# Kernel tuning notes

Measured on AMD Instinct MI355X. Metric: run time of the kernel, lower is better.

Reference implementation:

```python
import jax, jax.numpy as jnp
import numpy as np

DIM = 1024
HID = 2816  # int(2*4096/3)=2730 rounded up to multiple of 256
E = 2       # n_modalities
N = 32768   # tokens
EPS = 1e-5


def setup_inputs() -> dict:
    key = jax.random.key(0)
    ks = jax.random.split(key, 6)
    x = jax.random.normal(ks[0], (N, DIM), jnp.float32)
    # per-token modality label -> disjoint boolean masks [E, N]
    labels = jax.random.randint(ks[1], (N,), 0, E)
    modality_masks = labels[None, :] == jnp.arange(E)[:, None]
    s_in = 1.0 / np.sqrt(DIM)
    s_hid = 1.0 / np.sqrt(HID)
    # nn.Linear stores weight as [out_features, in_features]
    w1 = jax.random.normal(ks[2], (E, HID, DIM), jnp.float32) * s_in
    w3 = jax.random.normal(ks[3], (E, HID, DIM), jnp.float32) * s_in
    w2 = jax.random.normal(ks[4], (E, DIM, HID), jnp.float32) * s_hid
    norm_w = jnp.ones((E, DIM), jnp.float32)
    return {"x": x, "modality_masks": modality_masks,
            "w1": w1, "w3": w3, "w2": w2, "norm_w": norm_w}


def reference(x, modality_masks, w1, w3, w2, norm_w):
    # Each expert: SwiGLU FFN followed by RMSNorm (computed in fp32).
    def expert(W1, W3, W2, g):
        h = jax.nn.silu(x @ W1.T) * (x @ W3.T)   # [N, HID]
        o = h @ W2.T                              # [N, DIM]
        of = o.astype(jnp.float32)
        n = of * jax.lax.rsqrt(jnp.mean(of * of, axis=-1, keepdims=True) + EPS)
        return (n * g.astype(jnp.float32)).astype(o.dtype)

    outs = jax.vmap(expert)(w1, w3, w2, norm_w)   # [E, N, DIM]
    merged = jnp.zeros_like(x)
    for i in range(E - 1, -1, -1):
        merged = jnp.where(modality_masks[i][:, None], outs[i], merged)
    return merged
```

## Files before the change

kernel.cpp:

```cpp
#include <hip/hip_runtime.h>
#include <stdint.h>

#define DIM   1024
#define HID   2816
#define NEXP  2
#define NTOK  32768
#define RMS_EPS 1e-5f
#define NK1   16
#define NK2   44
#define NNT1  22
#define NNT2  4

typedef unsigned short u16;
typedef unsigned int   u32;
typedef __bf16 bf16_t;
typedef bf16_t bf16x8 __attribute__((ext_vector_type(8)));
typedef float  f32x4  __attribute__((ext_vector_type(4)));

#define BAR() asm volatile("s_barrier" ::: "memory")
#define WAIT6() asm volatile("s_waitcnt vmcnt(6)" ::: "memory")
#define WAIT0() asm volatile("s_waitcnt vmcnt(0)" ::: "memory")
#define MFMA_(a,b,c) __builtin_amdgcn_mfma_f32_16x16x32_bf16(a, b, c, 0, 0, 0)

__device__ __forceinline__ u16 f2bf(float f) {
  u32 u = __float_as_uint(f);
  u += 0x7FFFu + ((u >> 16) & 1u);
  return (u16)(u >> 16);
}

__device__ __forceinline__ void gld16(void* lds, const void* g) {
  __builtin_amdgcn_global_load_lds(
      (__attribute__((address_space(1))) void*)g,
      (__attribute__((address_space(3))) void*)lds, 16, 0, 0);
}

__device__ __forceinline__ int detect_layout(const u32* mi) {
  const int lane = threadIdx.x & 63;
  bool all01 = true, allf = true;
  for (int j = 0; j < 8; ++j) {
    u32 w = mi[j * 64 + lane];
    all01 &= (w <= 1u);
    allf  &= (w == 0u || w == 0x3F800000u);
  }
  unsigned long long b01 = __ballot(all01);
  unsigned long long bfl = __ballot(allf);
  if (b01 == ~0ull) return 0;
  if (bfl == ~0ull) return 1;
  return 2;
}

__device__ __forceinline__ bool mask_at(const void* m, int layout, int e, int n) {
  if (layout == 0) return ((const u32*)m)[e * NTOK + n] != 0u;
  if (layout == 1) return ((const float*)m)[e * NTOK + n] != 0.f;
  return ((const unsigned char*)m)[e * NTOK + n] != 0;
}

__device__ __forceinline__ int label_of(const void* m, int layout, int n) {
  for (int e = 0; e < NEXP; ++e)
    if (mask_at(m, layout, e, n)) return e;
  return 0;
}

__global__ __launch_bounds__(1024) void k_setup(const void* __restrict__ masks,
                                                int* __restrict__ meta,
                                                int* __restrict__ idx) {
  const int layout = detect_layout((const u32*)masks);
  const int t = threadIdx.x;
  const int base_n = t << 5;
  u32 bits = 0; int c0 = 0;
  for (int j = 0; j < 32; ++j) {
    const int l_ = label_of(masks, layout, base_n + j);
    bits |= ((u32)l_) << j;
    c0 += 1 - l_;
  }
  int inc = c0;
#pragma unroll
  for (int d = 1; d < 64; d <<= 1) {
    int v = __shfl_up(inc, d, 64);
    if ((t & 63) >= d) inc += v;
  }
  __shared__ int wsum[16];
  __shared__ int wexc[17];
  const int wv = t >> 6, ln = t & 63;
  if (ln == 63) wsum[wv] = inc;
  __syncthreads();
  if (t == 0) {
    int a = 0;
    for (int w = 0; w < 16; ++w) { wexc[w] = a; a += wsum[w]; }
    wexc[16] = a;
  }
  __syncthreads();
  const int cnt0 = wexc[16];
  int p0 = wexc[wv] + inc - c0;
  int p1 = cnt0 + base_n - p0;
  for (int j = 0; j < 32; ++j) {
    const int n = base_n + j;
    if ((bits >> j) & 1u) idx[p1++] = n;
    else                  idx[p0++] = n;
  }
  if (t == 0) { meta[0] = cnt0; meta[1] = NTOK - cnt0; }
}

__global__ void k_cvt(const float* __restrict__ in, u16* __restrict__ out, int n4) {
  const int stride = gridDim.x * blockDim.x;
  for (int i = blockIdx.x * blockDim.x + threadIdx.x; i < n4; i += stride) {
    const float4 v = ((const float4*)in)[i];
    ushort4 o;
    o.x = f2bf(v.x); o.y = f2bf(v.y); o.z = f2bf(v.z); o.w = f2bf(v.w);
    ((ushort4*)out)[i] = o;
  }
}

__global__ __launch_bounds__(256) void k_cvtx(const float* __restrict__ x,
                                              const int* __restrict__ idx,
                                              u16* __restrict__ xg) {
  const int r = blockIdx.x;
  const int tok = idx[r];
  const float4 v = ((const float4*)(x + ((size_t)tok << 10)))[threadIdx.x];
  ushort4 o;
  o.x = f2bf(v.x); o.y = f2bf(v.y); o.z = f2bf(v.z); o.w = f2bf(v.w);
  ((ushort4*)(xg + ((size_t)r << 10)))[threadIdx.x] = o;
}


#define ST1A(BUF, HH, P_, KT) {                                        \
    char* _d = (char*)&sA[BUF][(HH) * 8192] + t * 16;                  \
    gld16(_d,        ((HH) ? P_.a2 : P_.a0) + (size_t)(KT) * 64);      \
    gld16(_d + 8192, ((HH) ? P_.a3 : P_.a1) + (size_t)(KT) * 64); }

#define ST1B(BUF, HH, P_, KT) {                                                 \
    gld16((char*)&sB1[BUF][(HH) * 4096] + t * 16,                               \
          ((HH) ? P_.b11 : P_.b10) + (size_t)(KT) * 64);                        \
    gld16((char*)&sB3[BUF][(HH) * 4096] + t * 16,                               \
          ((HH) ? P_.b31 : P_.b30) + (size_t)(KT) * 64); }

#define G1_PH(MQ, NQ, ...) {                                                   \
    if ((MQ) == 0 && (NQ) == 0) {                                              \
      _Pragma("unroll") for (int q_ = 0; q_ < 2; ++q_) {                       \
        b1f0[q_] = *(const bf16x8*)&sB1c[bBase + q_*4096 + kb0];               \
        b1f1[q_] = *(const bf16x8*)&sB1c[bBase + q_*4096 + kb1];               \
        b3f0[q_] = *(const bf16x8*)&sB3c[bBase + q_*4096 + kb0];               \
        b3f1[q_] = *(const bf16x8*)&sB3c[bBase + q_*4096 + kb1];               \
      }                                                                        \
    }                                                                          \
    if ((NQ) == 0) {                                                           \
      _Pragma("unroll") for (int mi = 0; mi < 4; ++mi) {                       \
        af0[mi] = *(const bf16x8*)&sAc[aBase + (MQ)*8192 + mi*1024 + kb0];     \
        af1[mi] = *(const bf16x8*)&sAc[aBase + (MQ)*8192 + mi*1024 + kb1];     \
      }                                                                        \
    }                                                                          \
    __VA_ARGS__                                                                \
    BAR();                                                                     \
    __builtin_amdgcn_s_setprio(1);                                             \
    _Pragma("unroll") for (int mi = 0; mi < 4; ++mi) {                         \
      acc1[MQ][NQ][mi] = MFMA_(af0[mi], b1f0[NQ], acc1[MQ][NQ][mi]);           \
      acc3[MQ][NQ][mi] = MFMA_(af0[mi], b3f0[NQ], acc3[MQ][NQ][mi]);           \
      acc1[MQ][NQ][mi] = MFMA_(af1[mi], b1f1[NQ], acc1[MQ][NQ][mi]);           \
      acc3[MQ][NQ][mi] = MFMA_(af1[mi], b3f1[NQ], acc3[MQ][NQ][mi]);           \
    }                                                                          \
    __builtin_amdgcn_s_setprio(0);                                             \
  }

#define SETUP1(P_, IT) {                                                        \
    int _it = (IT);                                                            \
    int _m  = c + ((_it / NNT1) << 3);                                         \
    P_.nT   = _it % NNT1;                                                      \
    int _e  = _m >= nmt0;                                                      \
    P_.mT   = _e ? _m - nmt0 : _m;                                             \
    P_.cnt  = _e ? cnt1 : cnt0;                                                \
    P_.bas  = _e ? cnt0 : 0;                                                   \
    int _rg;                                                                   \
    _rg = P_.mT*256       + r0; _rg = _rg < P_.cnt ? _rg : P_.cnt-1;           \
    P_.a0 = xg + (size_t)(P_.bas+_rg)*DIM + srcoff;                            \
    _rg = P_.mT*256 +  64 + r0; _rg = _rg < P_.cnt ? _rg : P_.cnt-1;           \
    P_.a1 = xg + (size_t)(P_.bas+_rg)*DIM + srcoff;                            \
    _rg = P_.mT*256 + 128 + r0; _rg = _rg < P_.cnt ? _rg : P_.cnt-1;           \
    P_.a2 = xg + (size_t)(P_.bas+_rg)*DIM + srcoff;                            \
    _rg = P_.mT*256 + 192 + r0; _rg = _rg < P_.cnt ? _rg : P_.cnt-1;           \
    P_.a3 = xg + (size_t)(P_.bas+_rg)*DIM + srcoff;                            \
    size_t _o = ((size_t)_e * HID + (size_t)P_.nT * 128 + r0) * DIM + srcoff;  \
    P_.b10 = w1b + _o; P_.b11 = w1b + _o + (size_t)64 * DIM;                   \
    P_.b30 = w3b + _o; P_.b31 = w3b + _o + (size_t)64 * DIM; }

__global__ __launch_bounds__(512, 2) void k_gemm1(
    const u16* __restrict__ xg, const u16* __restrict__ w1b,
    const u16* __restrict__ w3b, const int* __restrict__ meta,
    u16* __restrict__ h)
{
  const int cnt0 = meta[0], cnt1 = meta[1];
  const int nmt0 = (cnt0 + 255) >> 8;
  const int nmt  = nmt0 + ((cnt1 + 255) >> 8);
  const int c = blockIdx.x & 7, q = blockIdx.x >> 3;
  const int mcnt  = (nmt > c) ? (((nmt - 1 - c) >> 3) + 1) : 0;
  const int items = mcnt * NNT1;
  int i = q;
  if (i >= items) return;

  __shared__ __attribute__((aligned(16))) u16 sA [2][256 * 64];
  __shared__ __attribute__((aligned(16))) u16 sB1[2][128 * 64];
  __shared__ __attribute__((aligned(16))) u16 sB3[2][128 * 64];

  const int t = threadIdx.x;
  const int srcoff = ((t & 7) ^ ((t >> 3) & 7)) * 8;
  const int r0 = t >> 3;
  const int wid = t >> 6, l = t & 63;
  const int wr = wid >> 2, wc = wid & 3;
  const int l15 = l & 15, lk = l >> 4, l7 = l & 7;
  const int kb0 = ((0 + lk) ^ l7) * 8;
  const int kb1 = ((4 + lk) ^ l7) * 8;
  const int aBase = (wr * 64 + l15) * 64;
  const int bBase = (wc * 16 + l15) * 64;

  struct P { const u16 *a0,*a1,*a2,*a3,*b10,*b11,*b30,*b31; int mT,cnt,bas,nT; };
  P cur, nxt;
  SETUP1(cur, i)
  bool hasN = (i + 32) < items;
  if (hasN) { SETUP1(nxt, i + 32) } else { nxt = cur; }

  f32x4 acc1[2][2][4] = {};
  f32x4 acc3[2][2][4] = {};
  bf16x8 af0[4], af1[4];
  bf16x8 b1f0[2], b1f1[2], b3f0[2], b3f1[2];

  ST1A(0, 0, cur, 0) ST1A(0, 1, cur, 0) ST1B(0, 0, cur, 0) ST1B(0, 1, cur, 0)
  ST1A(1, 0, cur, 1) ST1A(1, 1, cur, 1) ST1B(1, 0, cur, 1)
  WAIT6();
  BAR();

  for (;;) {
#pragma unroll 2
    for (int k = 0; k < NK1 - 2; ++k) {
      const u16* sAc  = &sA [k & 1][0];
      const u16* sB1c = &sB1[k & 1][0];
      const u16* sB3c = &sB3[k & 1][0];
      G1_PH(0, 0, ST1B((k & 1) ^ 1, 1, cur, k + 1))
      BAR();
      G1_PH(0, 1, ST1A(k & 1, 0, cur, k + 2))
      BAR();
      G1_PH(1, 0, )
      BAR();
      G1_PH(1, 1, ST1A(k & 1, 1, cur, k + 2) ST1B(k & 1, 0, cur, k + 2))
      WAIT6();
      BAR();
    }
    {
      const u16* sAc  = &sA [0][0];
      const u16* sB1c = &sB1[0][0];
      const u16* sB3c = &sB3[0][0];
      G1_PH(0, 0, ST1B(1, 1, cur, 15))
      BAR();
      G1_PH(0, 1, if (hasN) ST1A(0, 0, nxt, 0))
      BAR();
      G1_PH(1, 0, )
      BAR();
      G1_PH(1, 1, if (hasN) { ST1A(0, 1, nxt, 0) ST1B(0, 0, nxt, 0) })
      if (hasN) WAIT6(); else WAIT0();
      BAR();
    }
    {
      const u16* sAc  = &sA [1][0];
      const u16* sB1c = &sB1[1][0];
      const u16* sB3c = &sB3[1][0];
      G1_PH(0, 0, if (hasN) ST1B(0, 1, nxt, 0))
      BAR();
      G1_PH(0, 1, if (hasN) ST1A(1, 0, nxt, 1))
      BAR();
      G1_PH(1, 0, )
      BAR();
      G1_PH(1, 1, if (hasN) { ST1A(1, 1, nxt, 1) ST1B(1, 0, nxt, 1) })
      if (hasN) WAIT6();
      BAR();
    }

#pragma unroll
    for (int mq = 0; mq < 2; ++mq)
#pragma unroll
      for (int mi = 0; mi < 4; ++mi)
#pragma unroll
        for (int r = 0; r < 4; ++r) {
          const int lrow = mq * 128 + wr * 64 + mi * 16 + lk * 4 + r;
          const int rg = cur.mT * 256 + lrow;
          if (rg < cur.cnt) {
            u16* hrow = h + (size_t)(cur.bas + rg) * HID + cur.nT * 128 + wc * 16 + l15;
#pragma unroll
            for (int nq = 0; nq < 2; ++nq) {
              const float a = acc1[mq][nq][mi][r];
              const float b = acc3[mq][nq][mi][r];
              hrow[nq * 64] = f2bf((a / (1.f + __expf(-a))) * b);
            }
          }
        }

    if (!hasN) break;
    cur = nxt;
    i += 32;
    hasN = (i + 32) < items;
    if (hasN) SETUP1(nxt, i + 32)
#pragma unroll
    for (int a_ = 0; a_ < 2; ++a_)
#pragma unroll
      for (int b_ = 0; b_ < 2; ++b_)
#pragma unroll
        for (int m_ = 0; m_ < 4; ++m_) {
          acc1[a_][b_][m_] = (f32x4){0.f, 0.f, 0.f, 0.f};
          acc3[a_][b_][m_] = (f32x4){0.f, 0.f, 0.f, 0.f};
        }
  }
}


#define ST2A(BUF, HH, P_, KT) {                                        \
    char* _d = (char*)&sA[BUF][(HH) * 8192] + t * 16;                  \
    gld16(_d,        ((HH) ? P_.a2 : P_.a0) + (size_t)(KT) * 64);      \
    gld16(_d + 8192, ((HH) ? P_.a3 : P_.a1) + (size_t)(KT) * 64); }

#define ST2B(BUF, HH, P_, KT) {                                        \
    char* _d = (char*)&sB[BUF][(HH) * 8192] + t * 16;                  \
    gld16(_d,        ((HH) ? P_.b2 : P_.b0) + (size_t)(KT) * 64);      \
    gld16(_d + 8192, ((HH) ? P_.b3 : P_.b1) + (size_t)(KT) * 64); }

#define G2_PH(MQ, NQ, ...) {                                                   \
    if ((MQ) == 0 && (NQ) == 0) {                                              \
      _Pragma("unroll") for (int q_ = 0; q_ < 2; ++q_)                         \
        _Pragma("unroll") for (int ni = 0; ni < 2; ++ni) {                     \
          bf0[q_][ni] = *(const bf16x8*)&sBc[bBase + q_*8192 + ni*1024 + kb0]; \
          bf1[q_][ni] = *(const bf16x8*)&sBc[bBase + q_*8192 + ni*1024 + kb1]; \
        }                                                                      \
    }                                                                          \
    if ((NQ) == 0) {                                                           \
      _Pragma("unroll") for (int mi = 0; mi < 4; ++mi) {                       \
        af0[mi] = *(const bf16x8*)&sAc[aBase + (MQ)*8192 + mi*1024 + kb0];     \
        af1[mi] = *(const bf16x8*)&sAc[aBase + (MQ)*8192 + mi*1024 + kb1];     \
      }                                                                        \
    }                                                                          \
    __VA_ARGS__                                                                \
    BAR();                                                                     \
    __builtin_amdgcn_s_setprio(1);                                             \
    _Pragma("unroll") for (int mi = 0; mi < 4; ++mi)                           \
      _Pragma("unroll") for (int ni = 0; ni < 2; ++ni) {                       \
        acc[MQ][NQ][mi][ni] = MFMA_(af0[mi], bf0[NQ][ni], acc[MQ][NQ][mi][ni]);\
        acc[MQ][NQ][mi][ni] = MFMA_(af1[mi], bf1[NQ][ni], acc[MQ][NQ][mi][ni]);\
      }                                                                        \
    __builtin_amdgcn_s_setprio(0);                                             \
  }

#define SETUP2(P_, IT) {                                                        \
    int _it = (IT);                                                            \
    int _m  = c + ((_it >> 2) << 3);                                           \
    P_.nT   = _it & 3;                                                         \
    int _e  = _m >= nmt0;                                                      \
    P_.mT   = _e ? _m - nmt0 : _m;                                             \
    P_.cnt  = _e ? cnt1 : cnt0;                                                \
    P_.bas  = _e ? cnt0 : 0;                                                   \
    int _rg;                                                                   \
    _rg = P_.mT*256       + r0; _rg = _rg < P_.cnt ? _rg : P_.cnt-1;           \
    P_.a0 = hbuf + (size_t)(P_.bas+_rg)*HID + srcoff;                          \
    _rg = P_.mT*256 +  64 + r0; _rg = _rg < P_.cnt ? _rg : P_.cnt-1;           \
    P_.a1 = hbuf + (size_t)(P_.bas+_rg)*HID + srcoff;                          \
    _rg = P_.mT*256 + 128 + r0; _rg = _rg < P_.cnt ? _rg : P_.cnt-1;           \
    P_.a2 = hbuf + (size_t)(P_.bas+_rg)*HID + srcoff;                          \
    _rg = P_.mT*256 + 192 + r0; _rg = _rg < P_.cnt ? _rg : P_.cnt-1;           \
    P_.a3 = hbuf + (size_t)(P_.bas+_rg)*HID + srcoff;                          \
    size_t _wb = ((size_t)_e * DIM + (size_t)P_.nT * 256 + r0) * HID + srcoff; \
    P_.b0 = w2b + _wb;                                                         \
    P_.b1 = w2b + _wb + (size_t) 64 * HID;                                     \
    P_.b2 = w2b + _wb + (size_t)128 * HID;                                     \
    P_.b3 = w2b + _wb + (size_t)192 * HID; }

__global__ __launch_bounds__(512, 2) void k_gemm2(
    const u16* __restrict__ hbuf, const u16* __restrict__ w2b,
    const int* __restrict__ meta, const int* __restrict__ idx,
    float* __restrict__ out)
{
  const int cnt0 = meta[0], cnt1 = meta[1];
  const int nmt0 = (cnt0 + 255) >> 8;
  const int nmt  = nmt0 + ((cnt1 + 255) >> 8);
  const int c = blockIdx.x & 7, q = blockIdx.x >> 3;
  const int mcnt  = (nmt > c) ? (((nmt - 1 - c) >> 3) + 1) : 0;
  const int items = mcnt * NNT2;
  int i = q;
  if (i >= items) return;

  __shared__ __attribute__((aligned(16))) u16 sA[2][256 * 64];
  __shared__ __attribute__((aligned(16))) u16 sB[2][256 * 64];

  const int t = threadIdx.x;
  const int srcoff = ((t & 7) ^ ((t >> 3) & 7)) * 8;
  const int r0 = t >> 3;
  const int wid = t >> 6, l = t & 63;
  const int wr = wid >> 2, wc = wid & 3;
  const int l15 = l & 15, lk = l >> 4, l7 = l & 7;
  const int kb0 = ((0 + lk) ^ l7) * 8;
  const int kb1 = ((4 + lk) ^ l7) * 8;
  const int aBase = (wr * 64 + l15) * 64;
  const int bBase = (wc * 32 + l15) * 64;

  struct P { const u16 *a0,*a1,*a2,*a3,*b0,*b1,*b2,*b3; int mT,cnt,bas,nT; };
  P cur, nxt;
  SETUP2(cur, i)
  bool hasN = (i + 32) < items;
  if (hasN) { SETUP2(nxt, i + 32) } else { nxt = cur; }

  f32x4 acc[2][2][4][2] = {};
  bf16x8 af0[4], af1[4], bf0[2][2], bf1[2][2];

  ST2A(0, 0, cur, 0) ST2A(0, 1, cur, 0) ST2B(0, 0, cur, 0) ST2B(0, 1, cur, 0)
  ST2A(1, 0, cur, 1) ST2A(1, 1, cur, 1) ST2B(1, 0, cur, 1)
  WAIT6();
  BAR();

  for (;;) {
#pragma unroll 2
    for (int k = 0; k < NK2 - 2; ++k) {
      const u16* sAc = &sA[k & 1][0];
      const u16* sBc = &sB[k & 1][0];
      G2_PH(0, 0, ST2B((k & 1) ^ 1, 1, cur, k + 1))
      BAR();
      G2_PH(0, 1, ST2A(k & 1, 0, cur, k + 2))
      BAR();
      G2_PH(1, 0, )
      BAR();
      G2_PH(1, 1, ST2A(k & 1, 1, cur, k + 2) ST2B(k & 1, 0, cur, k + 2))
      WAIT6();
      BAR();
    }
    {
      const u16* sAc = &sA[0][0];
      const u16* sBc = &sB[0][0];
      G2_PH(0, 0, ST2B(1, 1, cur, NK2 - 1))
      BAR();
      G2_PH(0, 1, if (hasN) ST2A(0, 0, nxt, 0))
      BAR();
      G2_PH(1, 0, )
      BAR();
      G2_PH(1, 1, if (hasN) { ST2A(0, 1, nxt, 0) ST2B(0, 0, nxt, 0) })
      if (hasN) WAIT6(); else WAIT0();
      BAR();
    }
    {
      const u16* sAc = &sA[1][0];
      const u16* sBc = &sB[1][0];
      G2_PH(0, 0, if (hasN) ST2B(0, 1, nxt, 0))
      BAR();
      G2_PH(0, 1, if (hasN) ST2A(1, 0, nxt, 1))
      BAR();
      G2_PH(1, 0, )
      BAR();
      G2_PH(1, 1, if (hasN) { ST2A(1, 1, nxt, 1) ST2B(1, 0, nxt, 1) })
      if (hasN) WAIT6();
      BAR();
    }

#pragma unroll
    for (int mq = 0; mq < 2; ++mq)
#pragma unroll
      for (int mi = 0; mi < 4; ++mi)
#pragma unroll
        for (int r = 0; r < 4; ++r) {
          const int lrow = mq * 128 + wr * 64 + mi * 16 + lk * 4 + r;
          const int rg = cur.mT * 256 + lrow;
          if (rg < cur.cnt) {
            const int tok = idx[cur.bas + rg];
            float* orow = out + (size_t)tok * DIM + cur.nT * 256 + wc * 32 + l15;
#pragma unroll
            for (int nq = 0; nq < 2; ++nq)
#pragma unroll
              for (int ni = 0; ni < 2; ++ni)
                orow[nq * 128 + ni * 16] = acc[mq][nq][mi][ni][r];
          }
        }

    if (!hasN) break;
    cur = nxt;
    i += 32;
    hasN = (i + 32) < items;
    if (hasN) SETUP2(nxt, i + 32)
#pragma unroll
    for (int a_ = 0; a_ < 2; ++a_)
#pragma unroll
      for (int b_ = 0; b_ < 2; ++b_)
#pragma unroll
        for (int m_ = 0; m_ < 4; ++m_)
#pragma unroll
          for (int n_ = 0; n_ < 2; ++n_)
            acc[a_][b_][m_][n_] = (f32x4){0.f, 0.f, 0.f, 0.f};
  }
}

__global__ __launch_bounds__(256) void k_rms(
    float* __restrict__ out, const float* __restrict__ nw,
    const int* __restrict__ meta, const int* __restrict__ idx)
{
  const int wv = threadIdx.x >> 6, ln = threadIdx.x & 63;
  const int r = blockIdx.x * 4 + wv;
  const int e = (r >= meta[0]) ? 1 : 0;
  const int tok = idx[r];
  float* row = out + (size_t)tok * DIM;
  const float* g = nw + (size_t)e * DIM;

  float4 v[4];
  float ss = 0.f;
#pragma unroll
  for (int p = 0; p < 4; ++p) {
    v[p] = ((const float4*)row)[p * 64 + ln];
    ss += v[p].x * v[p].x + v[p].y * v[p].y + v[p].z * v[p].z + v[p].w * v[p].w;
  }
#pragma unroll
  for (int off = 32; off; off >>= 1) ss += __shfl_xor(ss, off, 64);
  const float sc = rsqrtf(ss * (1.0f / DIM) + RMS_EPS);
#pragma unroll
  for (int p = 0; p < 4; ++p) {
    const float4 gg = ((const float4*)g)[p * 64 + ln];
    v[p].x *= sc * gg.x; v[p].y *= sc * gg.y;
    v[p].z *= sc * gg.z; v[p].w *= sc * gg.w;
    ((float4*)row)[p * 64 + ln] = v[p];
  }
}

extern "C" void kernel_launch(void* const* d_in, const int* in_sizes, int n_in,
                              void* d_out, int out_size, void* d_ws, size_t ws_size,
                              hipStream_t stream)
{
  const float* x     = (const float*)d_in[0];
  const void*  masks = d_in[1];
  const float* w1    = (const float*)d_in[2];
  const float* w3    = (const float*)d_in[3];
  const float* w2    = (const float*)d_in[4];
  const float* nw    = (const float*)d_in[5];
  float* out = (float*)d_out;

  char* ws = (char*)d_ws;
  constexpr size_t OFF_IDX = 256;
  constexpr size_t OFF_XB  = OFF_IDX + (size_t)NTOK * 4;
  constexpr size_t OFF_W1B = OFF_XB + (size_t)NTOK * DIM * 2;
  constexpr size_t SZ_W    = (size_t)NEXP * HID * DIM * 2;
  constexpr size_t OFF_W3B = OFF_W1B + SZ_W;
  constexpr size_t OFF_W2B = OFF_W3B + SZ_W;
  constexpr size_t OFF_H   = OFF_W2B + SZ_W;

  int* meta = (int*)ws;
  int* idx  = (int*)(ws + OFF_IDX);
  u16* xg   = (u16*)(ws + OFF_XB);
  u16* w1b  = (u16*)(ws + OFF_W1B);
  u16* w3b  = (u16*)(ws + OFF_W3B);
  u16* w2b  = (u16*)(ws + OFF_W2B);
  u16* h    = (u16*)(ws + OFF_H);

  k_setup<<<1, 1024, 0, stream>>>(masks, meta, idx);

  const int wn4 = NEXP * HID * DIM / 4;
  k_cvt<<<2048, 256, 0, stream>>>(w1, w1b, wn4);
  k_cvt<<<2048, 256, 0, stream>>>(w3, w3b, wn4);
  k_cvt<<<2048, 256, 0, stream>>>(w2, w2b, wn4);
  k_cvtx<<<NTOK, 256, 0, stream>>>(x, idx, xg);

  k_gemm1<<<256, 512, 0, stream>>>(xg, w1b, w3b, meta, h);
  k_gemm2<<<256, 512, 0, stream>>>(h, w2b, meta, idx, out);
  k_rms<<<NTOK / 4, 256, 0, stream>>>(out, nw, meta, idx);
}
```

Measured before the change: 833.2 us.

## Switch both GEMMs to 32x32x16 MFMA with restructured fragment and prefetch schedule

Both grouped GEMM kernels now use the 32x32x16 bf16 MFMA instead of 16x16x32. The per-wave fragment layout, LDS read offsets, accumulator shapes and epilogue row/column mapping are rewritten to match. Global-to-LDS staging is split into quarter-tile loads spread across four phases, with adjusted vmcnt waits. The larger instruction is meant to cut MFMA issue count and LDS fragment reads per FLOP, at the cost of more accumulator registers and a riskier pipeline ordering.

```diff
diff --git a/kernel.cpp b/kernel.cpp
--- a/kernel.cpp
+++ b/kernel.cpp
@@ -15,12 +15,14 @@
 typedef unsigned int   u32;
 typedef __bf16 bf16_t;
 typedef bf16_t bf16x8 __attribute__((ext_vector_type(8)));
-typedef float  f32x4  __attribute__((ext_vector_type(4)));
-
-#define BAR() asm volatile("s_barrier" ::: "memory")
+typedef float  f32x16 __attribute__((ext_vector_type(16)));
+
+#define BAR()   asm volatile("s_barrier" ::: "memory")
+#define WAIT4() asm volatile("s_waitcnt vmcnt(4)" ::: "memory")
 #define WAIT6() asm volatile("s_waitcnt vmcnt(6)" ::: "memory")
+#define WAIT8() asm volatile("s_waitcnt vmcnt(8)" ::: "memory")
 #define WAIT0() asm volatile("s_waitcnt vmcnt(0)" ::: "memory")
-#define MFMA_(a,b,c) __builtin_amdgcn_mfma_f32_16x16x32_bf16(a, b, c, 0, 0, 0)
+#define M32(a,b,c) __builtin_amdgcn_mfma_f32_32x32x16_bf16(a, b, c, 0, 0, 0)
 
 __device__ __forceinline__ u16 f2bf(float f) {
   u32 u = __float_as_uint(f);
@@ -81,8 +83,8 @@
   }
   __shared__ int wsum[16];
   __shared__ int wexc[17];
-  const int wv = t >> 6, ln = t & 63;
-  if (ln == 63) wsum[wv] = inc;
+  const int wv = t >> 6;
+  if ((t & 63) == 63) wsum[wv] = inc;
   __syncthreads();
   if (t == 0) {
     int a = 0;
@@ -123,42 +125,53 @@
 }
 
 
-#define ST1A(BUF, HH, P_, KT) {                                        \
-    char* _d = (char*)&sA[BUF][(HH) * 8192] + t * 16;                  \
-    gld16(_d,        ((HH) ? P_.a2 : P_.a0) + (size_t)(KT) * 64);      \
-    gld16(_d + 8192, ((HH) ? P_.a3 : P_.a1) + (size_t)(KT) * 64); }
-
-#define ST1B(BUF, HH, P_, KT) {                                                 \
-    gld16((char*)&sB1[BUF][(HH) * 4096] + t * 16,                               \
-          ((HH) ? P_.b11 : P_.b10) + (size_t)(KT) * 64);                        \
-    gld16((char*)&sB3[BUF][(HH) * 4096] + t * 16,                               \
-          ((HH) ? P_.b31 : P_.b30) + (size_t)(KT) * 64); }
-
-#define G1_PH(MQ, NQ, ...) {                                                   \
-    if ((MQ) == 0 && (NQ) == 0) {                                              \
-      _Pragma("unroll") for (int q_ = 0; q_ < 2; ++q_) {                       \
-        b1f0[q_] = *(const bf16x8*)&sB1c[bBase + q_*4096 + kb0];               \
-        b1f1[q_] = *(const bf16x8*)&sB1c[bBase + q_*4096 + kb1];               \
-        b3f0[q_] = *(const bf16x8*)&sB3c[bBase + q_*4096 + kb0];               \
-        b3f1[q_] = *(const bf16x8*)&sB3c[bBase + q_*4096 + kb1];               \
-      }                                                                        \
-    }                                                                          \
-    if ((NQ) == 0) {                                                           \
-      _Pragma("unroll") for (int mi = 0; mi < 4; ++mi) {                       \
-        af0[mi] = *(const bf16x8*)&sAc[aBase + (MQ)*8192 + mi*1024 + kb0];     \
-        af1[mi] = *(const bf16x8*)&sAc[aBase + (MQ)*8192 + mi*1024 + kb1];     \
-      }                                                                        \
-    }                                                                          \
-    __VA_ARGS__                                                                \
-    BAR();                                                                     \
-    __builtin_amdgcn_s_setprio(1);                                             \
-    _Pragma("unroll") for (int mi = 0; mi < 4; ++mi) {                         \
-      acc1[MQ][NQ][mi] = MFMA_(af0[mi], b1f0[NQ], acc1[MQ][NQ][mi]);           \
-      acc3[MQ][NQ][mi] = MFMA_(af0[mi], b3f0[NQ], acc3[MQ][NQ][mi]);           \
-      acc1[MQ][NQ][mi] = MFMA_(af1[mi], b1f1[NQ], acc1[MQ][NQ][mi]);           \
-      acc3[MQ][NQ][mi] = MFMA_(af1[mi], b3f1[NQ], acc3[MQ][NQ][mi]);           \
-    }                                                                          \
-    __builtin_amdgcn_s_setprio(0);                                             \
+#define ST1A_Q(BUF, APTR, Q, KT) \
+    gld16((char*)&sA[BUF][(Q)*4096] + t*16, (APTR) + (size_t)(KT)*64);
+
+#define ST1B_H(BUF, HH, PB1, PB3, KT) {                                  \
+    gld16((char*)&sB1[BUF][(HH)*4096] + t*16, (PB1) + (size_t)(KT)*64);  \
+    gld16((char*)&sB3[BUF][(HH)*4096] + t*16, (PB3) + (size_t)(KT)*64); }
+
+#define G1_MFMA(RF, A0_, A1_, A2_, A3_)                                  \
+    acc1[RF] = M32(A0_, bh1[0], acc1[RF]);                               \
+    acc3[RF] = M32(A0_, bh3[0], acc3[RF]);                               \
+    acc1[RF] = M32(A1_, bh1[1], acc1[RF]);                               \
+    acc3[RF] = M32(A1_, bh3[1], acc3[RF]);                               \
+    acc1[RF] = M32(A2_, bh1[2], acc1[RF]);                               \
+    acc3[RF] = M32(A2_, bh3[2], acc3[RF]);                               \
+    acc1[RF] = M32(A3_, bh1[3], acc1[RF]);                               \
+    acc3[RF] = M32(A3_, bh3[3], acc3[RF]);
+
+#define G1_PH0(...) {                                                    \
+    bh1[0] = *(const bf16x8*)&sB1c[bb0];                                 \
+    bh1[1] = *(const bf16x8*)&sB1c[bb1];                                 \
+    bh1[2] = *(const bf16x8*)&sB1c[bb2];                                 \
+    bh1[3] = *(const bf16x8*)&sB1c[bb3];                                 \
+    bh3[0] = *(const bf16x8*)&sB3c[bb0];                                 \
+    bh3[1] = *(const bf16x8*)&sB3c[bb1];                                 \
+    bh3[2] = *(const bf16x8*)&sB3c[bb2];                                 \
+    bh3[3] = *(const bf16x8*)&sB3c[bb3];                                 \
+    bf16x8 a0_ = *(const bf16x8*)&sAc[av0];                              \
+    bf16x8 a1_ = *(const bf16x8*)&sAc[av1];                              \
+    bf16x8 a2_ = *(const bf16x8*)&sAc[av2];                              \
+    bf16x8 a3_ = *(const bf16x8*)&sAc[av3];                              \
+    __VA_ARGS__                                                          \
+    BAR();                                                               \
+    __builtin_amdgcn_s_setprio(1);                                       \
+    G1_MFMA(0, a0_, a1_, a2_, a3_)                                       \
+    __builtin_amdgcn_s_setprio(0);                                       \
+  }
+
+#define G1_PHX(RF, ...) {                                                \
+    bf16x8 a0_ = *(const bf16x8*)&sAc[av0 + (RF)*2048];                  \
+    bf16x8 a1_ = *(const bf16x8*)&sAc[av1 + (RF)*2048];                  \
+    bf16x8 a2_ = *(const bf16x8*)&sAc[av2 + (RF)*2048];                  \
+    bf16x8 a3_ = *(const bf16x8*)&sAc[av3 + (RF)*2048];                  \
+    __VA_ARGS__                                                          \
+    BAR();                                                               \
+    __builtin_amdgcn_s_setprio(1);                                       \
+    G1_MFMA(RF, a0_, a1_, a2_, a3_)                                      \
+    __builtin_amdgcn_s_setprio(0);                                       \
   }
 
 #define SETUP1(P_, IT) {                                                        \
@@ -205,11 +218,15 @@
   const int r0 = t >> 3;
   const int wid = t >> 6, l = t & 63;
   const int wr = wid >> 2, wc = wid & 3;
-  const int l15 = l & 15, lk = l >> 4, l7 = l & 7;
-  const int kb0 = ((0 + lk) ^ l7) * 8;
-  const int kb1 = ((4 + lk) ^ l7) * 8;
-  const int aBase = (wr * 64 + l15) * 64;
-  const int bBase = (wc * 16 + l15) * 64;
+  const int l31 = l & 31, h5 = l >> 5, l7 = l & 7;
+  const int ka0 = ((0 + h5) ^ l7) * 8;
+  const int ka1 = ((2 + h5) ^ l7) * 8;
+  const int ka2 = ((4 + h5) ^ l7) * 8;
+  const int ka3 = ((6 + h5) ^ l7) * 8;
+  const int aB = (wr * 128 + l31) * 64;
+  const int bB = (wc * 32 + l31) * 64;
+  const int av0 = aB + ka0, av1 = aB + ka1, av2 = aB + ka2, av3 = aB + ka3;
+  const int bb0 = bB + ka0, bb1 = bB + ka1, bb2 = bB + ka2, bb3 = bB + ka3;
 
   struct P { const u16 *a0,*a1,*a2,*a3,*b10,*b11,*b30,*b31; int mT,cnt,bas,nT; };
   P cur, nxt;
@@ -217,14 +234,16 @@
   bool hasN = (i + 32) < items;
   if (hasN) { SETUP1(nxt, i + 32) } else { nxt = cur; }
 
-  f32x4 acc1[2][2][4] = {};
-  f32x4 acc3[2][2][4] = {};
-  bf16x8 af0[4], af1[4];
-  bf16x8 b1f0[2], b1f1[2], b3f0[2], b3f1[2];
-
-  ST1A(0, 0, cur, 0) ST1A(0, 1, cur, 0) ST1B(0, 0, cur, 0) ST1B(0, 1, cur, 0)
-  ST1A(1, 0, cur, 1) ST1A(1, 1, cur, 1) ST1B(1, 0, cur, 1)
-  WAIT6();
+  f32x16 acc1[4] = {};
+  f32x16 acc3[4] = {};
+  bf16x8 bh1[4], bh3[4];
+
+  ST1B_H(0, 0, cur.b10, cur.b30, 0) ST1B_H(0, 1, cur.b11, cur.b31, 0)
+  ST1A_Q(0, cur.a0, 0, 0) ST1A_Q(0, cur.a1, 1, 0)
+  ST1A_Q(0, cur.a2, 2, 0) ST1A_Q(0, cur.a3, 3, 0)
+  ST1A_Q(1, cur.a0, 0, 1) ST1A_Q(1, cur.a2, 2, 1)
+  ST1B_H(1, 0, cur.b10, cur.b30, 1)
+  WAIT4();
   BAR();
 
   for (;;) {
@@ -233,13 +252,15 @@
       const u16* sAc  = &sA [k & 1][0];
       const u16* sB1c = &sB1[k & 1][0];
       const u16* sB3c = &sB3[k & 1][0];
-      G1_PH(0, 0, ST1B((k & 1) ^ 1, 1, cur, k + 1))
-      BAR();
-      G1_PH(0, 1, ST1A(k & 1, 0, cur, k + 2))
-      BAR();
-      G1_PH(1, 0, )
-      BAR();
-      G1_PH(1, 1, ST1A(k & 1, 1, cur, k + 2) ST1B(k & 1, 0, cur, k + 2))
+      const int cb = k & 1, nb = cb ^ 1;
+      G1_PH0(ST1B_H(nb, 1, cur.b11, cur.b31, k + 1))
+      BAR();
+      G1_PHX(1, ST1A_Q(nb, cur.a1, 1, k + 1) ST1A_Q(nb, cur.a3, 3, k + 1))
+      WAIT8();
+      BAR();
+      G1_PHX(2, ST1A_Q(cb, cur.a0, 0, k + 2) ST1A_Q(cb, cur.a2, 2, k + 2))
+      BAR();
+      G1_PHX(3, ST1B_H(cb, 0, cur.b10, cur.b30, k + 2))
       WAIT6();
       BAR();
     }
@@ -247,13 +268,14 @@
       const u16* sAc  = &sA [0][0];
       const u16* sB1c = &sB1[0][0];
       const u16* sB3c = &sB3[0][0];
-      G1_PH(0, 0, ST1B(1, 1, cur, 15))
-      BAR();
-      G1_PH(0, 1, if (hasN) ST1A(0, 0, nxt, 0))
-      BAR();
-      G1_PH(1, 0, )
-      BAR();
-      G1_PH(1, 1, if (hasN) { ST1A(0, 1, nxt, 0) ST1B(0, 0, nxt, 0) })
+      G1_PH0(ST1B_H(1, 1, cur.b11, cur.b31, NK1 - 1))
+      BAR();
+      G1_PHX(1, ST1A_Q(1, cur.a1, 1, NK1 - 1) ST1A_Q(1, cur.a3, 3, NK1 - 1))
+      WAIT8();
+      BAR();
+      G1_PHX(2, if (hasN) { ST1A_Q(0, nxt.a0, 0, 0) ST1A_Q(0, nxt.a2, 2, 0) })
+      BAR();
+      G1_PHX(3, if (hasN) ST1B_H(0, 0, nxt.b10, nxt.b30, 0))
       if (hasN) WAIT6(); else WAIT0();
       BAR();
     }
@@ -261,35 +283,34 @@
       const u16* sAc  = &sA [1][0];
       const u16* sB1c = &sB1[1][0];
       const u16* sB3c = &sB3[1][0];
-      G1_PH(0, 0, if (hasN) ST1B(0, 1, nxt, 0))
-      BAR();
-      G1_PH(0, 1, if (hasN) ST1A(1, 0, nxt, 1))
-      BAR();
-      G1_PH(1, 0, )
-      BAR();
-      G1_PH(1, 1, if (hasN) { ST1A(1, 1, nxt, 1) ST1B(1, 0, nxt, 1) })
+      G1_PH0(if (hasN) ST1B_H(0, 1, nxt.b11, nxt.b31, 0))
+      BAR();
+      G1_PHX(1, if (hasN) { ST1A_Q(0, nxt.a1, 1, 0) ST1A_Q(0, nxt.a3, 3, 0) })
+      WAIT8();
+      BAR();
+      G1_PHX(2, if (hasN) { ST1A_Q(1, nxt.a0, 0, 1) ST1A_Q(1, nxt.a2, 2, 1) })
+      BAR();
+      G1_PHX(3, if (hasN) { ST1B_H(1, 0, nxt.b10, nxt.b30, 1) })
       if (hasN) WAIT6();
       BAR();
     }
 
-#pragma unroll
-    for (int mq = 0; mq < 2; ++mq)
-#pragma unroll
-      for (int mi = 0; mi < 4; ++mi)
-#pragma unroll
-        for (int r = 0; r < 4; ++r) {
-          const int lrow = mq * 128 + wr * 64 + mi * 16 + lk * 4 + r;
+    {
+      const int colo = cur.nT * 128 + wc * 32 + l31;
+#pragma unroll
+      for (int rf = 0; rf < 4; ++rf)
+#pragma unroll
+        for (int r = 0; r < 16; ++r) {
+          const int lrow = wr * 128 + rf * 32 + (r & 3) + 8 * (r >> 2) + 4 * h5;
           const int rg = cur.mT * 256 + lrow;
           if (rg < cur.cnt) {
-            u16* hrow = h + (size_t)(cur.bas + rg) * HID + cur.nT * 128 + wc * 16 + l15;
-#pragma unroll
-            for (int nq = 0; nq < 2; ++nq) {
-              const float a = acc1[mq][nq][mi][r];
-              const float b = acc3[mq][nq][mi][r];
-              hrow[nq * 64] = f2bf((a / (1.f + __expf(-a))) * b);
-            }
+            const float a = acc1[rf][r];
+            const float b = acc3[rf][r];
+            h[(size_t)(cur.bas + rg) * HID + colo] =
+                f2bf((a / (1.f + __expf(-a))) * b);
           }
         }
+    }
 
     if (!hasN) break;
     cur = nxt;
@@ -297,51 +318,63 @@
     hasN = (i + 32) < items;
     if (hasN) SETUP1(nxt, i + 32)
 #pragma unroll
-    for (int a_ = 0; a_ < 2; ++a_)
-#pragma unroll
-      for (int b_ = 0; b_ < 2; ++b_)
-#pragma unroll
-        for (int m_ = 0; m_ < 4; ++m_) {
-          acc1[a_][b_][m_] = (f32x4){0.f, 0.f, 0.f, 0.f};
-          acc3[a_][b_][m_] = (f32x4){0.f, 0.f, 0.f, 0.f};
-        }
-  }
-}
-
-
-#define ST2A(BUF, HH, P_, KT) {                                        \
-    char* _d = (char*)&sA[BUF][(HH) * 8192] + t * 16;                  \
-    gld16(_d,        ((HH) ? P_.a2 : P_.a0) + (size_t)(KT) * 64);      \
-    gld16(_d + 8192, ((HH) ? P_.a3 : P_.a1) + (size_t)(KT) * 64); }
-
-#define ST2B(BUF, HH, P_, KT) {                                        \
-    char* _d = (char*)&sB[BUF][(HH) * 8192] + t * 16;                  \
-    gld16(_d,        ((HH) ? P_.b2 : P_.b0) + (size_t)(KT) * 64);      \
-    gld16(_d + 8192, ((HH) ? P_.b3 : P_.b1) + (size_t)(KT) * 64); }
-
-#define G2_PH(MQ, NQ, ...) {                                                   \
-    if ((MQ) == 0 && (NQ) == 0) {                                              \
-      _Pragma("unroll") for (int q_ = 0; q_ < 2; ++q_)                         \
-        _Pragma("unroll") for (int ni = 0; ni < 2; ++ni) {                     \
-          bf0[q_][ni] = *(const bf16x8*)&sBc[bBase + q_*8192 + ni*1024 + kb0]; \
-          bf1[q_][ni] = *(const bf16x8*)&sBc[bBase + q_*8192 + ni*1024 + kb1]; \
-        }                                                                      \
-    }                                                                          \
-    if ((NQ) == 0) {                                                           \
-      _Pragma("unroll") for (int mi = 0; mi < 4; ++mi) {                       \
-        af0[mi] = *(const bf16x8*)&sAc[aBase + (MQ)*8192 + mi*1024 + kb0];     \
-        af1[mi] = *(const bf16x8*)&sAc[aBase + (MQ)*8192 + mi*1024 + kb1];     \
-      }                                                                        \
-    }                                                                          \
-    __VA_ARGS__                                                                \
-    BAR();                                                                     \
-    __builtin_amdgcn_s_setprio(1);                                             \
-    _Pragma("unroll") for (int mi = 0; mi < 4; ++mi)                           \
-      _Pragma("unroll") for (int ni = 0; ni < 2; ++ni) {                       \
-        acc[MQ][NQ][mi][ni] = MFMA_(af0[mi], bf0[NQ][ni], acc[MQ][NQ][mi][ni]);\
-        acc[MQ][NQ][mi][ni] = MFMA_(af1[mi], bf1[NQ][ni], acc[MQ][NQ][mi][ni]);\
-      }                                                                        \
-    __builtin_amdgcn_s_setprio(0);                                             \
+    for (int m_ = 0; m_ < 4; ++m_)
+#pragma unroll
+      for (int j_ = 0; j_ < 16; ++j_) {
+        acc1[m_][j_] = 0.f;
+        acc3[m_][j_] = 0.f;
+      }
+  }
+}
+
+
+#define ST2A_Q(BUF, APTR, Q, KT) \
+    gld16((char*)&sA[BUF][(Q)*4096] + t*16, (APTR) + (size_t)(KT)*64);
+
+#define ST2B_H(BUF, HH, PBL, PBH, KT) {                                        \
+    gld16((char*)&sB[BUF][(HH)*8192] + t*16,        (PBL) + (size_t)(KT)*64);  \
+    gld16((char*)&sB[BUF][(HH)*8192 + 4096] + t*16, (PBH) + (size_t)(KT)*64); }
+
+#define G2_MFMA(RF, A0_, A1_, A2_, A3_)                                  \
+    acc[RF][0] = M32(A0_, bhA[0], acc[RF][0]);                           \
+    acc[RF][1] = M32(A0_, bhB[0], acc[RF][1]);                           \
+    acc[RF][0] = M32(A1_, bhA[1], acc[RF][0]);                           \
+    acc[RF][1] = M32(A1_, bhB[1], acc[RF][1]);                           \
+    acc[RF][0] = M32(A2_, bhA[2], acc[RF][0]);                           \
+    acc[RF][1] = M32(A2_, bhB[2], acc[RF][1]);                           \
+    acc[RF][0] = M32(A3_, bhA[3], acc[RF][0]);                           \
+    acc[RF][1] = M32(A3_, bhB[3], acc[RF][1]);
+
+#define G2_PH0(...) {                                                    \
+    bhA[0] = *(const bf16x8*)&sBc[bb0];                                  \
+    bhA[1] = *(const bf16x8*)&sBc[bb1];                                  \
+    bhA[2] = *(const bf16x8*)&sBc[bb2];                                  \
+    bhA[3] = *(const bf16x8*)&sBc[bb3];                                  \
+    bhB[0] = *(const bf16x8*)&sBc[bb0 + 2048];                           \
+    bhB[1] = *(const bf16x8*)&sBc[bb1 + 2048];                           \
+    bhB[2] = *(const bf16x8*)&sBc[bb2 + 2048];                           \
+    bhB[3] = *(const bf16x8*)&sBc[bb3 + 2048];                           \
+    bf16x8 a0_ = *(const bf16x8*)&sAc[av0];                              \
+    bf16x8 a1_ = *(const bf16x8*)&sAc[av1];                              \
+    bf16x8 a2_ = *(const bf16x8*)&sAc[av2];                              \
+    bf16x8 a3_ = *(const bf16x8*)&sAc[av3];                              \
+    __VA_ARGS__                                                          \
+    BAR();                                                               \
+    __builtin_amdgcn_s_setprio(1);                                       \
+    G2_MFMA(0, a0_, a1_, a2_, a3_)                                       \
+    __builtin_amdgcn_s_setprio(0);                                       \
+  }
+
+#define G2_PHX(RF, ...) {                                                \
+    bf16x8 a0_ = *(const bf16x8*)&sAc[av0 + (RF)*2048];                  \
+    bf16x8 a1_ = *(const bf16x8*)&sAc[av1 + (RF)*2048];                  \
+    bf16x8 a2_ = *(const bf16x8*)&sAc[av2 + (RF)*2048];                  \
+    bf16x8 a3_ = *(const bf16x8*)&sAc[av3 + (RF)*2048];                  \
+    __VA_ARGS__                                                          \
+    BAR();                                                               \
+    __builtin_amdgcn_s_setprio(1);                                       \
+    G2_MFMA(RF, a0_, a1_, a2_, a3_)                                      \
+    __builtin_amdgcn_s_setprio(0);                                       \
   }
 
 #define SETUP2(P_, IT) {                                                        \
@@ -389,11 +422,15 @@
   const int r0 = t >> 3;
   const int wid = t >> 6, l = t & 63;
   const int wr = wid >> 2, wc = wid & 3;
-  const int l15 = l & 15, lk = l >> 4, l7 = l & 7;
-  const int kb0 = ((0 + lk) ^ l7) * 8;
-  const int kb1 = ((4 + lk) ^ l7) * 8;
-  const int aBase = (wr * 64 + l15) * 64;
-  const int bBase = (wc * 32 + l15) * 64;
+  const int l31 = l & 31, h5 = l >> 5, l7 = l & 7;
+  const int ka0 = ((0 + h5) ^ l7) * 8;
+  const int ka1 = ((2 + h5) ^ l7) * 8;
+  const int ka2 = ((4 + h5) ^ l7) * 8;
+  const int ka3 = ((6 + h5) ^ l7) * 8;
+  const int aB = (wr * 128 + l31) * 64;
+  const int bB = (wc * 64 + l31) * 64;
+  const int av0 = aB + ka0, av1 = aB + ka1, av2 = aB + ka2, av3 = aB + ka3;
+  const int bb0 = bB + ka0, bb1 = bB + ka1, bb2 = bB + ka2, bb3 = bB + ka3;
 
   struct P { const u16 *a0,*a1,*a2,*a3,*b0,*b1,*b2,*b3; int mT,cnt,bas,nT; };
   P cur, nxt;
@@ -401,12 +438,15 @@
   bool hasN = (i + 32) < items;
   if (hasN) { SETUP2(nxt, i + 32) } else { nxt = cur; }
 
-  f32x4 acc[2][2][4][2] = {};
-  bf16x8 af0[4], af1[4], bf0[2][2], bf1[2][2];
-
-  ST2A(0, 0, cur, 0) ST2A(0, 1, cur, 0) ST2B(0, 0, cur, 0) ST2B(0, 1, cur, 0)
-  ST2A(1, 0, cur, 1) ST2A(1, 1, cur, 1) ST2B(1, 0, cur, 1)
-  WAIT6();
+  f32x16 acc[4][2] = {};
+  bf16x8 bhA[4], bhB[4];
+
+  ST2B_H(0, 0, cur.b0, cur.b1, 0) ST2B_H(0, 1, cur.b2, cur.b3, 0)
+  ST2A_Q(0, cur.a0, 0, 0) ST2A_Q(0, cur.a1, 1, 0)
+  ST2A_Q(0, cur.a2, 2, 0) ST2A_Q(0, cur.a3, 3, 0)
+  ST2A_Q(1, cur.a0, 0, 1) ST2A_Q(1, cur.a2, 2, 1)
+  ST2B_H(1, 0, cur.b0, cur.b1, 1)
+  WAIT4();
   BAR();
 
   for (;;) {
@@ -414,61 +454,63 @@
     for (int k = 0; k < NK2 - 2; ++k) {
       const u16* sAc = &sA[k & 1][0];
       const u16* sBc = &sB[k & 1][0];
-      G2_PH(0, 0, ST2B((k & 1) ^ 1, 1, cur, k + 1))
-      BAR();
-      G2_PH(0, 1, ST2A(k & 1, 0, cur, k + 2))
-      BAR();
-      G2_PH(1, 0, )
-      BAR();
-      G2_PH(1, 1, ST2A(k & 1, 1, cur, k + 2) ST2B(k & 1, 0, cur, k + 2))
+      const int cb = k & 1, nb = cb ^ 1;
+      G2_PH0(ST2B_H(nb, 1, cur.b2, cur.b3, k + 1))
+      BAR();
+      G2_PHX(1, ST2A_Q(nb, cur.a1, 1, k + 1) ST2A_Q(nb, cur.a3, 3, k + 1))
+      WAIT8();
+      BAR();
+      G2_PHX(2, ST2A_Q(cb, cur.a0, 0, k + 2) ST2A_Q(cb, cur.a2, 2, k + 2))
+      BAR();
+      G2_PHX(3, ST2B_H(cb, 0, cur.b0, cur.b1, k + 2))
       WAIT6();
       BAR();
     }
     {
       const u16* sAc = &sA[0][0];
       const u16* sBc = &sB[0][0];
-      G2_PH(0, 0, ST2B(1, 1, cur, NK2 - 1))
-      BAR();
-      G2_PH(0, 1, if (hasN) ST2A(0, 0, nxt, 0))
-      BAR();
-      G2_PH(1, 0, )
-      BAR();
-      G2_PH(1, 1, if (hasN) { ST2A(0, 1, nxt, 0) ST2B(0, 0, nxt, 0) })
+      G2_PH0(ST2B_H(1, 1, cur.b2, cur.b3, NK2 - 1))
+      BAR();
+      G2_PHX(1, ST2A_Q(1, cur.a1, 1, NK2 - 1) ST2A_Q(1, cur.a3, 3, NK2 - 1))
+      WAIT8();
+      BAR();
+      G2_PHX(2, if (hasN) { ST2A_Q(0, nxt.a0, 0, 0) ST2A_Q(0, nxt.a2, 2, 0) })
+      BAR();
+      G2_PHX(3, if (hasN) ST2B_H(0, 0, nxt.b0, nxt.b1, 0))
       if (hasN) WAIT6(); else WAIT0();
       BAR();
     }
     {
       const u16* sAc = &sA[1][0];
       const u16* sBc = &sB[1][0];
-      G2_PH(0, 0, if (hasN) ST2B(0, 1, nxt, 0))
-      BAR();
-      G2_PH(0, 1, if (hasN) ST2A(1, 0, nxt, 1))
-      BAR();
-      G2_PH(1, 0, )
-      BAR();
-      G2_PH(1, 1, if (hasN) { ST2A(1, 1, nxt, 1) ST2B(1, 0, nxt, 1) })
+      G2_PH0(if (hasN) ST2B_H(0, 1, nxt.b2, nxt.b3, 0))
+      BAR();
+      G2_PHX(1, if (hasN) { ST2A_Q(0, nxt.a1, 1, 0) ST2A_Q(0, nxt.a3, 3, 0) })
+      WAIT8();
+      BAR();
+      G2_PHX(2, if (hasN) { ST2A_Q(1, nxt.a0, 0, 1) ST2A_Q(1, nxt.a2, 2, 1) })
+      BAR();
+      G2_PHX(3, if (hasN) { ST2B_H(1, 0, nxt.b0, nxt.b1, 1) })
       if (hasN) WAIT6();
       BAR();
     }
 
-#pragma unroll
-    for (int mq = 0; mq < 2; ++mq)
-#pragma unroll
-      for (int mi = 0; mi < 4; ++mi)
-#pragma unroll
-        for (int r = 0; r < 4; ++r) {
-          const int lrow = mq * 128 + wr * 64 + mi * 16 + lk * 4 + r;
+    {
+      const int colo = cur.nT * 256 + wc * 64 + l31;
+#pragma unroll
+      for (int rf = 0; rf < 4; ++rf)
+#pragma unroll
+        for (int r = 0; r < 16; ++r) {
+          const int lrow = wr * 128 + rf * 32 + (r & 3) + 8 * (r >> 2) + 4 * h5;
           const int rg = cur.mT * 256 + lrow;
           if (rg < cur.cnt) {
             const int tok = idx[cur.bas + rg];
-            float* orow = out + (size_t)tok * DIM + cur.nT * 256 + wc * 32 + l15;
-#pragma unroll
-            for (int nq = 0; nq < 2; ++nq)
-#pragma unroll
-              for (int ni = 0; ni < 2; ++ni)
-                orow[nq * 128 + ni * 16] = acc[mq][nq][mi][ni][r];
+            float* orow = out + (size_t)tok * DIM + colo;
+            orow[0]  = acc[rf][0][r];
+            orow[32] = acc[rf][1][r];
           }
         }
+    }
 
     if (!hasN) break;
     cur = nxt;
@@ -476,14 +518,12 @@
     hasN = (i + 32) < items;
     if (hasN) SETUP2(nxt, i + 32)
 #pragma unroll
-    for (int a_ = 0; a_ < 2; ++a_)
-#pragma unroll
-      for (int b_ = 0; b_ < 2; ++b_)
-#pragma unroll
-        for (int m_ = 0; m_ < 4; ++m_)
-#pragma unroll
-          for (int n_ = 0; n_ < 2; ++n_)
-            acc[a_][b_][m_][n_] = (f32x4){0.f, 0.f, 0.f, 0.f};
+    for (int m_ = 0; m_ < 4; ++m_)
+#pragma unroll
+      for (int j_ = 0; j_ < 16; ++j_) {
+        acc[m_][0][j_] = 0.f;
+        acc[m_][1][j_] = 0.f;
+      }
   }
 }
 
```

New measurement: 911.2 us. 1.09x slower.

## Load B fragments per phase, reorder tile traversal, relax launch bounds

Applied to the files above, without the earlier changes.

Both GEMM kernels now read B fragments from LDS in every phase instead of loading all of them up front, which shrinks the B register arrays. The work-item mapping is reordered so consecutive items walk M tiles within one N tile (nT = it / mcnt), changing which weight and activation tiles are reused across blocks in L2. Launch bounds are relaxed from 2 to 1 blocks per SM, which gives the compiler more registers and may lower occupancy. The extra LDS reads per phase add latency before the MFMAs.

```diff
diff --git a/kernel.cpp b/kernel.cpp
--- a/kernel.cpp
+++ b/kernel.cpp
@@ -81,8 +81,8 @@
   }
   __shared__ int wsum[16];
   __shared__ int wexc[17];
-  const int wv = t >> 6, ln = t & 63;
-  if (ln == 63) wsum[wv] = inc;
+  const int wv = t >> 6;
+  if ((t & 63) == 63) wsum[wv] = inc;
   __syncthreads();
   if (t == 0) {
     int a = 0;
@@ -135,36 +135,34 @@
           ((HH) ? P_.b31 : P_.b30) + (size_t)(KT) * 64); }
 
 #define G1_PH(MQ, NQ, ...) {                                                   \
-    if ((MQ) == 0 && (NQ) == 0) {                                              \
-      _Pragma("unroll") for (int q_ = 0; q_ < 2; ++q_) {                       \
-        b1f0[q_] = *(const bf16x8*)&sB1c[bBase + q_*4096 + kb0];               \
-        b1f1[q_] = *(const bf16x8*)&sB1c[bBase + q_*4096 + kb1];               \
-        b3f0[q_] = *(const bf16x8*)&sB3c[bBase + q_*4096 + kb0];               \
-        b3f1[q_] = *(const bf16x8*)&sB3c[bBase + q_*4096 + kb1];               \
-      }                                                                        \
-    }                                                                          \
     if ((NQ) == 0) {                                                           \
       _Pragma("unroll") for (int mi = 0; mi < 4; ++mi) {                       \
         af0[mi] = *(const bf16x8*)&sAc[aBase + (MQ)*8192 + mi*1024 + kb0];     \
         af1[mi] = *(const bf16x8*)&sAc[aBase + (MQ)*8192 + mi*1024 + kb1];     \
       }                                                                        \
     }                                                                          \
+    b1f0 = *(const bf16x8*)&sB1c[bBase + (NQ)*4096 + kb0];                     \
+    b1f1 = *(const bf16x8*)&sB1c[bBase + (NQ)*4096 + kb1];                     \
+    b3f0 = *(const bf16x8*)&sB3c[bBase + (NQ)*4096 + kb0];                     \
+    b3f1 = *(const bf16x8*)&sB3c[bBase + (NQ)*4096 + kb1];                     \
     __VA_ARGS__                                                                \
     BAR();                                                                     \
     __builtin_amdgcn_s_setprio(1);                                             \
     _Pragma("unroll") for (int mi = 0; mi < 4; ++mi) {                         \
-      acc1[MQ][NQ][mi] = MFMA_(af0[mi], b1f0[NQ], acc1[MQ][NQ][mi]);           \
-      acc3[MQ][NQ][mi] = MFMA_(af0[mi], b3f0[NQ], acc3[MQ][NQ][mi]);           \
-      acc1[MQ][NQ][mi] = MFMA_(af1[mi], b1f1[NQ], acc1[MQ][NQ][mi]);           \
-      acc3[MQ][NQ][mi] = MFMA_(af1[mi], b3f1[NQ], acc3[MQ][NQ][mi]);           \
+      acc1[MQ][NQ][mi] = MFMA_(af0[mi], b1f0, acc1[MQ][NQ][mi]);               \
+      acc3[MQ][NQ][mi] = MFMA_(af0[mi], b3f0, acc3[MQ][NQ][mi]);               \
+      acc1[MQ][NQ][mi] = MFMA_(af1[mi], b1f1, acc1[MQ][NQ][mi]);               \
+      acc3[MQ][NQ][mi] = MFMA_(af1[mi], b3f1, acc3[MQ][NQ][mi]);               \
     }                                                                          \
     __builtin_amdgcn_s_setprio(0);                                             \
   }
 
 #define SETUP1(P_, IT) {                                                        \
     int _it = (IT);                                                            \
-    int _m  = c + ((_it / NNT1) << 3);                                         \
-    P_.nT   = _it % NNT1;                                                      \
+    int _nt = _it / mcnt;                                                      \
+    int _j  = _it - _nt * mcnt;                                                \
+    int _m  = c + (_j << 3);                                                   \
+    P_.nT   = _nt;                                                             \
     int _e  = _m >= nmt0;                                                      \
     P_.mT   = _e ? _m - nmt0 : _m;                                             \
     P_.cnt  = _e ? cnt1 : cnt0;                                                \
@@ -182,7 +180,7 @@
     P_.b10 = w1b + _o; P_.b11 = w1b + _o + (size_t)64 * DIM;                   \
     P_.b30 = w3b + _o; P_.b31 = w3b + _o + (size_t)64 * DIM; }
 
-__global__ __launch_bounds__(512, 2) void k_gemm1(
+__global__ __launch_bounds__(512, 1) void k_gemm1(
     const u16* __restrict__ xg, const u16* __restrict__ w1b,
     const u16* __restrict__ w3b, const int* __restrict__ meta,
     u16* __restrict__ h)
@@ -219,8 +217,7 @@
 
   f32x4 acc1[2][2][4] = {};
   f32x4 acc3[2][2][4] = {};
-  bf16x8 af0[4], af1[4];
-  bf16x8 b1f0[2], b1f1[2], b3f0[2], b3f1[2];
+  bf16x8 af0[4], af1[4], b1f0, b1f1, b3f0, b3f1;
 
   ST1A(0, 0, cur, 0) ST1A(0, 1, cur, 0) ST1B(0, 0, cur, 0) ST1B(0, 1, cur, 0)
   ST1A(1, 0, cur, 1) ST1A(1, 1, cur, 1) ST1B(1, 0, cur, 1)
@@ -320,34 +317,33 @@
     gld16(_d + 8192, ((HH) ? P_.b3 : P_.b1) + (size_t)(KT) * 64); }
 
 #define G2_PH(MQ, NQ, ...) {                                                   \
-    if ((MQ) == 0 && (NQ) == 0) {                                              \
-      _Pragma("unroll") for (int q_ = 0; q_ < 2; ++q_)                         \
-        _Pragma("unroll") for (int ni = 0; ni < 2; ++ni) {                     \
-          bf0[q_][ni] = *(const bf16x8*)&sBc[bBase + q_*8192 + ni*1024 + kb0]; \
-          bf1[q_][ni] = *(const bf16x8*)&sBc[bBase + q_*8192 + ni*1024 + kb1]; \
-        }                                                                      \
-    }                                                                          \
     if ((NQ) == 0) {                                                           \
       _Pragma("unroll") for (int mi = 0; mi < 4; ++mi) {                       \
         af0[mi] = *(const bf16x8*)&sAc[aBase + (MQ)*8192 + mi*1024 + kb0];     \
         af1[mi] = *(const bf16x8*)&sAc[aBase + (MQ)*8192 + mi*1024 + kb1];     \
       }                                                                        \
     }                                                                          \
+    _Pragma("unroll") for (int ni = 0; ni < 2; ++ni) {                         \
+      bf0[ni] = *(const bf16x8*)&sBc[bBase + (NQ)*8192 + ni*1024 + kb0];       \
+      bf1[ni] = *(const bf16x8*)&sBc[bBase + (NQ)*8192 + ni*1024 + kb1];       \
+    }                                                                          \
     __VA_ARGS__                                                                \
     BAR();                                                                     \
     __builtin_amdgcn_s_setprio(1);                                             \
     _Pragma("unroll") for (int mi = 0; mi < 4; ++mi)                           \
       _Pragma("unroll") for (int ni = 0; ni < 2; ++ni) {                       \
-        acc[MQ][NQ][mi][ni] = MFMA_(af0[mi], bf0[NQ][ni], acc[MQ][NQ][mi][ni]);\
-        acc[MQ][NQ][mi][ni] = MFMA_(af1[mi], bf1[NQ][ni], acc[MQ][NQ][mi][ni]);\
+        acc[MQ][NQ][mi][ni] = MFMA_(af0[mi], bf0[ni], acc[MQ][NQ][mi][ni]);    \
+        acc[MQ][NQ][mi][ni] = MFMA_(af1[mi], bf1[ni], acc[MQ][NQ][mi][ni]);    \
       }                                                                        \
     __builtin_amdgcn_s_setprio(0);                                             \
   }
 
 #define SETUP2(P_, IT) {                                                        \
     int _it = (IT);                                                            \
-    int _m  = c + ((_it >> 2) << 3);                                           \
-    P_.nT   = _it & 3;                                                         \
+    int _nt = _it / mcnt;                                                      \
+    int _j  = _it - _nt * mcnt;                                                \
+    int _m  = c + (_j << 3);                                                   \
+    P_.nT   = _nt;                                                             \
     int _e  = _m >= nmt0;                                                      \
     P_.mT   = _e ? _m - nmt0 : _m;                                             \
     P_.cnt  = _e ? cnt1 : cnt0;                                                \
@@ -367,7 +363,7 @@
     P_.b2 = w2b + _wb + (size_t)128 * HID;                                     \
     P_.b3 = w2b + _wb + (size_t)192 * HID; }
 
-__global__ __launch_bounds__(512, 2) void k_gemm2(
+__global__ __launch_bounds__(512, 1) void k_gemm2(
     const u16* __restrict__ hbuf, const u16* __restrict__ w2b,
     const int* __restrict__ meta, const int* __restrict__ idx,
     float* __restrict__ out)
@@ -402,7 +398,7 @@
   if (hasN) { SETUP2(nxt, i + 32) } else { nxt = cur; }
 
   f32x4 acc[2][2][4][2] = {};
-  bf16x8 af0[4], af1[4], bf0[2][2], bf1[2][2];
+  bf16x8 af0[4], af1[4], bf0[2], bf1[2];
 
   ST2A(0, 0, cur, 0) ST2A(0, 1, cur, 0) ST2B(0, 0, cur, 0) ST2B(0, 1, cur, 0)
   ST2A(1, 0, cur, 1) ST2A(1, 1, cur, 1) ST2B(1, 0, cur, 1)
```

New measurement: 820.8 us. About the same (-1.5%).
